# Optimization experiments

Hardware: AMD Instinct MI355X
Metric: run time of the kernel (lower is better)

Reference implementation:

```python
import jax, jax.numpy as jnp
import numpy as np


def _gcn_layer(x, W, b, row, col, num_nodes):
    # x: [N, F_in]; W: [F_in, F_out]; row/col: [E2] (with self-loops appended)
    xw = x @ W  # [N, F_out]
    ones = jnp.ones(row.shape[0], dtype=xw.dtype)
    deg = jax.ops.segment_sum(ones, col, num_segments=num_nodes)  # in-degree incl. self-loop
    dinv = jnp.where(deg > 0, jax.lax.rsqrt(deg), 0.0)
    norm = dinv[row] * dinv[col]  # [E2]
    msg = xw[row] * norm[:, None]  # gather + per-edge scale
    out = jax.ops.segment_sum(msg, col, num_segments=num_nodes)  # scatter-add to targets
    return out + b


def setup_inputs() -> dict:
    key = jax.random.key(0)
    k1, k2, k3, k4, k5 = jax.random.split(key, 5)
    N, E, F_in, F_hid = 100000, 640000, 128, 128
    x = jax.random.normal(k1, (N, F_in), dtype=jnp.float32)
    edge_index = jax.random.randint(k2, (2, E), 0, N, dtype=jnp.int64)
    # Glorot-style init like PyG GCNConv
    s1 = (6.0 / (F_in + F_hid)) ** 0.5
    W1 = jax.random.uniform(k3, (F_in, F_hid), jnp.float32, -s1, s1)
    b1 = jnp.zeros((F_hid,), jnp.float32)
    s2 = (6.0 / (F_hid + F_hid)) ** 0.5
    W2 = jax.random.uniform(k4, (F_hid, F_hid), jnp.float32, -s2, s2)
    b2 = jnp.zeros((F_hid,), jnp.float32)
    return {"x": x, "edge_index": edge_index, "W1": W1, "b1": b1, "W2": W2, "b2": b2}


def reference(x, edge_index, W1, b1, W2, b2):
    N = x.shape[0]
    # GCN adds self-loops before symmetric normalization (add_self_loops=True default)
    self_idx = jnp.arange(N, dtype=edge_index.dtype)
    row = jnp.concatenate([edge_index[0], self_idx])
    col = jnp.concatenate([edge_index[1], self_idx])
    h = _gcn_layer(x, W1, b1, row, col, N)
    h = jax.nn.relu(h)
    # dropout is identity in eval mode (training=False)
    out = _gcn_layer(h, W2, b2, row, col, N)
    return out
```

## Files before the change

### kernel.cpp

```cpp
#include <hip/hip_runtime.h>
#include <cstdint>
#include <cstddef>


typedef unsigned int u32;
typedef unsigned short u16;
typedef __attribute__((ext_vector_type(8))) short short8;
typedef __attribute__((ext_vector_type(4))) float f32x4;

__device__ __forceinline__ float bf2f(u32 lo16) {
  union { u32 u; float f; } c; c.u = lo16 << 16; return c.f;
}
__device__ __forceinline__ u32 f2bf(float f) {
  union { float f; u32 u; } c; c.f = f;
  return (c.u + 0x7fffu + ((c.u >> 16) & 1u)) >> 16;
}

__global__ __launch_bounds__(256) void zero_wt_kernel(
    const float* __restrict__ W1, const float* __restrict__ W2,
    u16* __restrict__ Wt1, u16* __restrict__ Wt2,
    u16* __restrict__ s1, u16* __restrict__ hp,
    int* __restrict__ cnt, int N) {
  int gt = blockIdx.x * 256 + threadIdx.x;
  if (gt < N) cnt[gt] = 0;
  if (gt < 32768) {
    const float* W = (gt < 16384) ? W1 : W2;
    u16* Wt = (gt < 16384) ? Wt1 : Wt2;
    int idx = gt & 16383;
    Wt[(idx & 127) * 128 + (idx >> 7)] = (u16)f2bf(W[idx]);
  }
  if (gt < 16) {
    ((uint4*)(s1 + (size_t)N * 128))[gt] = make_uint4(0, 0, 0, 0);
    ((uint4*)(hp + (size_t)N * 128))[gt] = make_uint4(0, 0, 0, 0);
  }
}

__global__ __launch_bounds__(256) void count_kernel(
    const int* __restrict__ cols, const int* __restrict__ rows,
    int* __restrict__ cnt, int E, int N) {
  int e = blockIdx.x * 256 + threadIdx.x;
  if (e >= E) return;
  int c = cols[e];
  int r = rows[e];
  if ((unsigned)c >= (unsigned)N || (unsigned)r >= (unsigned)N) return;
  atomicAdd(&cnt[c], 1);
}

__global__ __launch_bounds__(256) void scan1_kernel(
    const int* __restrict__ cnt, int* __restrict__ rowptr,
    int* __restrict__ bsum, float* __restrict__ dinv, int N) {
  __shared__ int sd[256];
  int t = threadIdx.x;
  int base = blockIdx.x * 1024 + t * 4;
  int c0 = (base + 0 < N) ? cnt[base + 0] : 0;
  int c1 = (base + 1 < N) ? cnt[base + 1] : 0;
  int c2 = (base + 2 < N) ? cnt[base + 2] : 0;
  int c3 = (base + 3 < N) ? cnt[base + 3] : 0;
  if (base + 0 < N) dinv[base + 0] = rsqrtf((float)c0 + 1.0f);
  if (base + 1 < N) dinv[base + 1] = rsqrtf((float)c1 + 1.0f);
  if (base + 2 < N) dinv[base + 2] = rsqrtf((float)c2 + 1.0f);
  if (base + 3 < N) dinv[base + 3] = rsqrtf((float)c3 + 1.0f);
  int s = c0 + c1 + c2 + c3;
  sd[t] = s;
  __syncthreads();
  for (int off = 1; off < 256; off <<= 1) {
    int v = (t >= off) ? sd[t - off] : 0;
    __syncthreads();
    sd[t] += v;
    __syncthreads();
  }
  int excl = sd[t] - s;
  if (base + 0 < N) rowptr[base + 0] = excl;
  if (base + 1 < N) rowptr[base + 1] = excl + c0;
  if (base + 2 < N) rowptr[base + 2] = excl + c0 + c1;
  if (base + 3 < N) rowptr[base + 3] = excl + c0 + c1 + c2;
  if (t == 255) bsum[blockIdx.x] = sd[255];
}

__global__ __launch_bounds__(128) void scan2_kernel(
    const int* __restrict__ bsum, int* __restrict__ bsum2,
    int* __restrict__ rowptr, int NB, int N) {
  __shared__ int sd[128];
  int t = threadIdx.x;
  int v = (t < NB) ? bsum[t] : 0;
  sd[t] = v;
  __syncthreads();
  for (int off = 1; off < 128; off <<= 1) {
    int u = (t >= off) ? sd[t - off] : 0;
    __syncthreads();
    sd[t] += u;
    __syncthreads();
  }
  bsum2[t] = sd[t] - v;
  if (t == NB - 1) rowptr[N] = sd[t];
}

__global__ __launch_bounds__(256) void finalize_kernel(
    const float* __restrict__ x, const float* __restrict__ dinv,
    int* __restrict__ rowptr, const int* __restrict__ bsum2,
    u16* __restrict__ s1, int N, int NB) {
  int b = blockIdx.x, t = threadIdx.x;
  if (b < NB) {
    int base = b * 1024 + t * 4;
    int add = bsum2[b];
#pragma unroll
    for (int k = 0; k < 4; k++)
      if (base + k < N) rowptr[base + k] += add;
  }
  int total = N * 16;
  for (int idx = b * 256 + t; idx < total; idx += gridDim.x * 256) {
    int node = idx >> 4, l = idx & 15;
    float di = dinv[node];
    const float* xp = x + (size_t)node * 128 + l * 8;
    float4 v0 = *(const float4*)xp;
    float4 v1 = *(const float4*)(xp + 4);
    uint4 p;
    p.x = f2bf(di * v0.x) | (f2bf(di * v0.y) << 16);
    p.y = f2bf(di * v0.z) | (f2bf(di * v0.w) << 16);
    p.z = f2bf(di * v1.x) | (f2bf(di * v1.y) << 16);
    p.w = f2bf(di * v1.z) | (f2bf(di * v1.w) << 16);
    ((uint4*)s1)[idx] = p;
  }
}

__global__ __launch_bounds__(256) void fill_kernel(
    const int* __restrict__ cols, const int* __restrict__ rows,
    const int* __restrict__ rowptr, int* __restrict__ cnt,
    int* __restrict__ adj, int E, int N) {
  int e = blockIdx.x * 256 + threadIdx.x;
  if (e >= E) return;
  int c = cols[e];
  int r = rows[e];
  if ((unsigned)c >= (unsigned)N || (unsigned)r >= (unsigned)N) return;
  int pos = atomicSub(&cnt[c], 1) - 1;
  if (pos >= 0) adj[rowptr[c] + pos] = r;
}

template <int LAYER>
__global__ __launch_bounds__(256) void fused_ag_kernel(
    const uint4* __restrict__ src, const int* __restrict__ rowptr,
    const int* __restrict__ adj, const float* __restrict__ dinv,
    const float* __restrict__ bias, const uint4* __restrict__ Wt,
    void* __restrict__ out, int N) {
  __shared__ __align__(16) u16 smem[128 * 136 + 64 * 136];
  __shared__ float dv_s[64];
  u16 (*Ws)[136] = (u16(*)[136])smem;
  u16 (*Gs)[136] = (u16(*)[136])(smem + 128 * 136);
  const int tid = threadIdx.x;
  const int row0 = blockIdx.x * 64;

#pragma unroll
  for (int i = 0; i < 8; i++) {
    int linear = tid + i * 256;
    int n = linear >> 4, kq = linear & 15;
    *(uint4*)&Ws[n][kq * 8] = Wt[linear];
  }

  const int qw = tid >> 4;
  const int l = tid & 15;
#pragma unroll
  for (int pass = 0; pass < 4; ++pass) {
    int lrow = pass * 16 + qw;
    int node = row0 + lrow;
    float a[8] = {0.f, 0.f, 0.f, 0.f, 0.f, 0.f, 0.f, 0.f};
    float di = 0.f;
    if (node < N) {
      di = dinv[node];
      uint4 sv = src[(size_t)node * 16 + l];
      a[0] = bf2f(sv.x & 0xffff); a[1] = bf2f(sv.x >> 16);
      a[2] = bf2f(sv.y & 0xffff); a[3] = bf2f(sv.y >> 16);
      a[4] = bf2f(sv.z & 0xffff); a[5] = bf2f(sv.z >> 16);
      a[6] = bf2f(sv.w & 0xffff); a[7] = bf2f(sv.w >> 16);
      int beg = rowptr[node], end = rowptr[node + 1];
      for (int j = beg; j < end; j += 8) {
        int sidx[8];
#pragma unroll
        for (int k = 0; k < 8; k++) {
          int jj = j + k;
          sidx[k] = (jj < end) ? adj[jj] : N;
        }
        uint4 v[8];
#pragma unroll
        for (int k = 0; k < 8; k++) v[k] = src[(size_t)sidx[k] * 16 + l];
#pragma unroll
        for (int k = 0; k < 8; k++) {
          a[0] += bf2f(v[k].x & 0xffff); a[1] += bf2f(v[k].x >> 16);
          a[2] += bf2f(v[k].y & 0xffff); a[3] += bf2f(v[k].y >> 16);
          a[4] += bf2f(v[k].z & 0xffff); a[5] += bf2f(v[k].z >> 16);
          a[6] += bf2f(v[k].w & 0xffff); a[7] += bf2f(v[k].w >> 16);
        }
      }
    }
    uint4 p;
    p.x = f2bf(di * a[0]) | (f2bf(di * a[1]) << 16);
    p.y = f2bf(di * a[2]) | (f2bf(di * a[3]) << 16);
    p.z = f2bf(di * a[4]) | (f2bf(di * a[5]) << 16);
    p.w = f2bf(di * a[6]) | (f2bf(di * a[7]) << 16);
    *(uint4*)&Gs[lrow][l * 8] = p;
    if (l == 0) dv_s[lrow] = di;
  }
  __syncthreads();

  const int wave = tid >> 6, lane = tid & 63;
  const int lm = lane & 15, quad = lane >> 4;
  const int m0 = wave * 16;
  f32x4 acc[8];
#pragma unroll
  for (int nt = 0; nt < 8; nt++) acc[nt] = (f32x4){0.f, 0.f, 0.f, 0.f};
#pragma unroll
  for (int k0 = 0; k0 < 128; k0 += 32) {
    short8 afrag = *(const short8*)&Gs[m0 + lm][k0 + quad * 8];
#pragma unroll
    for (int nt = 0; nt < 8; nt++) {
      short8 bfrag = *(const short8*)&Ws[nt * 16 + lm][k0 + quad * 8];
      acc[nt] = __builtin_amdgcn_mfma_f32_16x16x32_bf16(afrag, bfrag, acc[nt], 0, 0, 0);
    }
  }

  float bv[8];
#pragma unroll
  for (int nt = 0; nt < 8; nt++) bv[nt] = bias[nt * 16 + lm];

  __syncthreads();
  if (LAYER == 1) {
    int rbase = m0 + quad * 4;
#pragma unroll
    for (int r = 0; r < 4; r++) {
      int lrow = rbase + r;
      float dv = dv_s[lrow];
#pragma unroll
      for (int nt = 0; nt < 8; nt++) {
        float v = fmaxf(acc[nt][r] + bv[nt], 0.f);
        Gs[lrow][nt * 16 + lm] = (u16)f2bf(v * dv);
      }
    }
    __syncthreads();
    u16* C = (u16*)out;
#pragma unroll
    for (int i = 0; i < 4; i++) {
      int linear = tid + i * 256;
      int row = linear >> 4, c8 = linear & 15;
      int grow = row0 + row;
      if (grow < N)
        *(uint4*)(C + (size_t)grow * 128 + c8 * 8) = *(const uint4*)&Gs[row][c8 * 8];
    }
  } else {
    float (*Fs)[132] = (float(*)[132])smem;
    int rbase = m0 + quad * 4;
#pragma unroll
    for (int r = 0; r < 4; r++) {
      int lrow = rbase + r;
#pragma unroll
      for (int nt = 0; nt < 8; nt++)
        Fs[lrow][nt * 16 + lm] = acc[nt][r] + bv[nt];
    }
    __syncthreads();
    float* C = (float*)out;
#pragma unroll
    for (int i = 0; i < 8; i++) {
      int linear = tid + i * 256;
      int row = linear >> 5, c4 = linear & 31;
      int grow = row0 + row;
      if (grow < N) {
        f32x4 v = *(const f32x4*)&Fs[row][c4 * 4];
        __builtin_nontemporal_store(v, (f32x4*)(C + (size_t)grow * 128 + c4 * 4));
      }
    }
  }
}

extern "C" void kernel_launch(void* const* d_in, const int* in_sizes, int n_in,
                              void* d_out, int out_size, void* d_ws, size_t ws_size,
                              hipStream_t stream) {
  const float* x  = (const float*)d_in[0];
  const int*   ei = (const int*)d_in[1];
  const float* W1 = (const float*)d_in[2];
  const float* b1 = (const float*)d_in[3];
  const float* W2 = (const float*)d_in[4];
  const float* b2 = (const float*)d_in[5];
  float* out = (float*)d_out;

  const int F = 128;
  const int N = in_sizes[0] / F;
  const int E = in_sizes[1] / 2;
  const int* rows = ei;
  const int* cols = ei + E;

  u16*   Wt1    = (u16*)d_ws;
  u16*   Wt2    = Wt1 + 128 * 128;
  u16*   s1     = Wt2 + 128 * 128;
  u16*   hp     = s1 + (size_t)(N + 1) * F;
  float* dinv   = (float*)(hp + (size_t)(N + 1) * F);
  int*   cnt    = (int*)(dinv + N);
  int*   rowptr = cnt + N;
  int*   adj    = rowptr + (N + 1);
  int*   bsum   = adj + E;
  int*   bsum2  = bsum + 128;

  const int NB = (N + 1023) / 1024;
  int eblocks = (E + 255) / 256;
  int nblocks = (N + 255) / 256;
  int fblocks = (NB > 784) ? NB : 784;

  zero_wt_kernel<<<nblocks, 256, 0, stream>>>(W1, W2, Wt1, Wt2, s1, hp, cnt, N);
  count_kernel<<<eblocks, 256, 0, stream>>>(cols, rows, cnt, E, N);
  scan1_kernel<<<NB, 256, 0, stream>>>(cnt, rowptr, bsum, dinv, N);
  scan2_kernel<<<1, 128, 0, stream>>>(bsum, bsum2, rowptr, NB, N);
  finalize_kernel<<<fblocks, 256, 0, stream>>>(x, dinv, rowptr, bsum2, s1, N, NB);
  fill_kernel<<<eblocks, 256, 0, stream>>>(cols, rows, rowptr, cnt, adj, E, N);

  int gblocks = (N + 63) / 64;
  fused_ag_kernel<1><<<gblocks, 256, 0, stream>>>(
      (const uint4*)s1, rowptr, adj, dinv, b1, (const uint4*)Wt1, hp, N);
  fused_ag_kernel<2><<<gblocks, 256, 0, stream>>>(
      (const uint4*)hp, rowptr, adj, dinv, b2, (const uint4*)Wt2, out, N);
}
```

Measured before the change: 260.2 us.

## Read MFMA weight fragments from global memory and store layer-2 output directly

```diff
diff --git a/kernel.cpp b/kernel.cpp
--- a/kernel.cpp
+++ b/kernel.cpp
@@ -140,21 +140,12 @@
 __global__ __launch_bounds__(256) void fused_ag_kernel(
     const uint4* __restrict__ src, const int* __restrict__ rowptr,
     const int* __restrict__ adj, const float* __restrict__ dinv,
-    const float* __restrict__ bias, const uint4* __restrict__ Wt,
+    const float* __restrict__ bias, const u16* __restrict__ Wt,
     void* __restrict__ out, int N) {
-  __shared__ __align__(16) u16 smem[128 * 136 + 64 * 136];
+  __shared__ __align__(16) u16 Gs[64][136];
   __shared__ float dv_s[64];
-  u16 (*Ws)[136] = (u16(*)[136])smem;
-  u16 (*Gs)[136] = (u16(*)[136])(smem + 128 * 136);
   const int tid = threadIdx.x;
   const int row0 = blockIdx.x * 64;
-
-#pragma unroll
-  for (int i = 0; i < 8; i++) {
-    int linear = tid + i * 256;
-    int n = linear >> 4, kq = linear & 15;
-    *(uint4*)&Ws[n][kq * 8] = Wt[linear];
-  }
 
   const int qw = tid >> 4;
   const int l = tid & 15;
@@ -204,25 +195,28 @@
   const int wave = tid >> 6, lane = tid & 63;
   const int lm = lane & 15, quad = lane >> 4;
   const int m0 = wave * 16;
+  const u16* wbase = Wt + lm * 128 + quad * 8;
   f32x4 acc[8];
 #pragma unroll
   for (int nt = 0; nt < 8; nt++) acc[nt] = (f32x4){0.f, 0.f, 0.f, 0.f};
 #pragma unroll
   for (int k0 = 0; k0 < 128; k0 += 32) {
     short8 afrag = *(const short8*)&Gs[m0 + lm][k0 + quad * 8];
-#pragma unroll
-    for (int nt = 0; nt < 8; nt++) {
-      short8 bfrag = *(const short8*)&Ws[nt * 16 + lm][k0 + quad * 8];
-      acc[nt] = __builtin_amdgcn_mfma_f32_16x16x32_bf16(afrag, bfrag, acc[nt], 0, 0, 0);
-    }
+    short8 bfrag[8];
+#pragma unroll
+    for (int nt = 0; nt < 8; nt++)
+      bfrag[nt] = *(const short8*)(wbase + nt * 2048 + k0);
+#pragma unroll
+    for (int nt = 0; nt < 8; nt++)
+      acc[nt] = __builtin_amdgcn_mfma_f32_16x16x32_bf16(afrag, bfrag[nt], acc[nt], 0, 0, 0);
   }
 
   float bv[8];
 #pragma unroll
   for (int nt = 0; nt < 8; nt++) bv[nt] = bias[nt * 16 + lm];
 
-  __syncthreads();
   if (LAYER == 1) {
+    __syncthreads();
     int rbase = m0 + quad * 4;
 #pragma unroll
     for (int r = 0; r < 4; r++) {
@@ -245,25 +239,15 @@
         *(uint4*)(C + (size_t)grow * 128 + c8 * 8) = *(const uint4*)&Gs[row][c8 * 8];
     }
   } else {
-    float (*Fs)[132] = (float(*)[132])smem;
-    int rbase = m0 + quad * 4;
+    float* C = (float*)out;
 #pragma unroll
     for (int r = 0; r < 4; r++) {
-      int lrow = rbase + r;
-#pragma unroll
-      for (int nt = 0; nt < 8; nt++)
-        Fs[lrow][nt * 16 + lm] = acc[nt][r] + bv[nt];
-    }
-    __syncthreads();
-    float* C = (float*)out;
-#pragma unroll
-    for (int i = 0; i < 8; i++) {
-      int linear = tid + i * 256;
-      int row = linear >> 5, c4 = linear & 31;
-      int grow = row0 + row;
+      int grow = row0 + m0 + quad * 4 + r;
       if (grow < N) {
-        f32x4 v = *(const f32x4*)&Fs[row][c4 * 4];
-        __builtin_nontemporal_store(v, (f32x4*)(C + (size_t)grow * 128 + c4 * 4));
+        float* Cp = C + (size_t)grow * 128 + lm;
+#pragma unroll
+        for (int nt = 0; nt < 8; nt++)
+          __builtin_nontemporal_store(acc[nt][r] + bv[nt], Cp + nt * 16);
       }
     }
   }
@@ -311,7 +295,7 @@
 
   int gblocks = (N + 63) / 64;
   fused_ag_kernel<1><<<gblocks, 256, 0, stream>>>(
-      (const uint4*)s1, rowptr, adj, dinv, b1, (const uint4*)Wt1, hp, N);
+      (const uint4*)s1, rowptr, adj, dinv, b1, Wt1, hp, N);
   fused_ag_kernel<2><<<gblocks, 256, 0, stream>>>(
-      (const uint4*)hp, rowptr, adj, dinv, b2, (const uint4*)Wt2, out, N);
-}
+      (const uint4*)hp, rowptr, adj, dinv, b2, Wt2, out, N);
+}
```

New measurement: 281.8 us. +8.3%, slower.
